# Performance work log

Measured on AMD Instinct MI355X. Metric: run time of the kernel, lower is better.

The kernel has to match this reference:

```python
import jax, jax.numpy as jnp
import numpy as np

EPS = 1e-5


def _in_relu(y):
    # instance norm (no affine, biased var, eps=1e-5) + ReLU, y: [B,C,H,W]
    mu = jnp.mean(y, axis=(-2, -1), keepdims=True)
    var = jnp.mean((y - mu) ** 2, axis=(-2, -1), keepdims=True)
    return jax.nn.relu((y - mu) * jax.lax.rsqrt(var + EPS))


def _conv3(x, w, b):
    # x: [C,H,W], w: [O,I,3,3] -> [O,H,W]
    y = jax.lax.conv_general_dilated(x[None], w, (1, 1), ((1, 1), (1, 1)),
                                     dimension_numbers=('NCHW', 'OIHW', 'NCHW'))[0]
    return y + b[:, None, None]


def _mod_block(x, W, b, mod):
    # per-sample weight modulation: mod[n] * W, then conv+IN+relu; x: [B,C,H,W], mod: [B,O,I,3,3]
    y = jax.vmap(lambda xi, mi: _conv3(xi, mi * W, b))(x, mod)
    return _in_relu(y)


def _maxpool2(x):
    return jax.lax.reduce_window(x, -jnp.inf, jax.lax.max, (1, 1, 2, 2), (1, 1, 2, 2), 'VALID')


def _up2(x):
    B, C, H, W = x.shape
    # bilinear, half-pixel centers == PyTorch align_corners=False
    return jax.image.resize(x, (B, C, 2 * H, 2 * W), method='bilinear')


def _conv1x1(x, w, b):
    y = jax.lax.conv_general_dilated(x, w, (1, 1), 'VALID',
                                     dimension_numbers=('NCHW', 'OIHW', 'NCHW'))
    return y + b[None, :, None, None]


def setup_inputs() -> dict:
    key = jax.random.key(0)
    B, H, W = 8, 256, 256
    ks = iter(jax.random.split(key, 64))
    d = {}
    d['us_query_input'] = jax.random.normal(next(ks), (B, 1, H, W), jnp.float32)
    d['ksp_query_imgs'] = jax.random.normal(next(ks), (B, H, W, 2), jnp.float32)
    d['ksp_mask_query'] = jax.random.uniform(next(ks), (B, H, W), jnp.float32)
    down_io = [(1, 32), (32, 64), (64, 128), (128, 256)]
    up_io = [(512, 128), (256, 64), (128, 32), (64, 32)]
    for i, (ci, co) in enumerate(down_io):
        d[f'down_mod_{i}'] = jax.random.normal(next(ks), (B, co, ci, 3, 3), jnp.float32)
        d[f'W_d{i}'] = 0.05 * jax.random.normal(next(ks), (co, ci, 3, 3), jnp.float32)
        d[f'b_d{i}'] = 0.05 * jax.random.normal(next(ks), (co,), jnp.float32)
    d['latent_mod'] = jax.random.normal(next(ks), (B, 256, 256, 3, 3), jnp.float32)
    d['W_lat'] = 0.05 * jax.random.normal(next(ks), (256, 256, 3, 3), jnp.float32)
    d['b_lat'] = 0.05 * jax.random.normal(next(ks), (256,), jnp.float32)
    for i, (ci, co) in enumerate(up_io):
        d[f'up_mod_{i}'] = jax.random.normal(next(ks), (B, co, ci, 3, 3), jnp.float32)
        d[f'W_u{i}'] = 0.05 * jax.random.normal(next(ks), (co, ci, 3, 3), jnp.float32)
        d[f'b_u{i}'] = 0.05 * jax.random.normal(next(ks), (co,), jnp.float32)
    d['w_c1'] = 0.05 * jax.random.normal(next(ks), (16, 32, 1, 1), jnp.float32)
    d['b_c1'] = 0.05 * jax.random.normal(next(ks), (16,), jnp.float32)
    d['w_c2'] = 0.05 * jax.random.normal(next(ks), (1, 16, 1, 1), jnp.float32)
    d['b_c2'] = 0.05 * jax.random.normal(next(ks), (1,), jnp.float32)
    d['w_c3'] = 0.05 * jax.random.normal(next(ks), (1, 1, 1, 1), jnp.float32)
    d['b_c3'] = 0.05 * jax.random.normal(next(ks), (1,), jnp.float32)
    return d


def reference(us_query_input, ksp_query_imgs, ksp_mask_query,
              down_mod_0, down_mod_1, down_mod_2, down_mod_3,
              latent_mod, up_mod_0, up_mod_1, up_mod_2, up_mod_3,
              W_d0, b_d0, W_d1, b_d1, W_d2, b_d2, W_d3, b_d3,
              W_lat, b_lat,
              W_u0, b_u0, W_u1, b_u1, W_u2, b_u2, W_u3, b_u3,
              w_c1, b_c1, w_c2, b_c2, w_c3, b_c3):
    x0 = us_query_input
    out = x0
    skips = []
    downs = [(W_d0, b_d0, down_mod_0), (W_d1, b_d1, down_mod_1),
             (W_d2, b_d2, down_mod_2), (W_d3, b_d3, down_mod_3)]
    for Wc, bc, m in downs:
        out = _mod_block(out, Wc, bc, m)
        skips.append(out)
        out = _maxpool2(out)
    out = _mod_block(out, W_lat, b_lat, latent_mod)
    ups = [(W_u0, b_u0, up_mod_0), (W_u1, b_u1, up_mod_1),
           (W_u2, b_u2, up_mod_2), (W_u3, b_u3, up_mod_3)]
    for Wc, bc, m in ups:
        out = _up2(out)
        out = jnp.concatenate([out, skips.pop()], axis=1)
        out = _mod_block(out, Wc, bc, m)
    out = _conv1x1(_conv1x1(_conv1x1(out, w_c1, b_c1), w_c2, b_c2), w_c3, b_c3)
    out = out + x0
    # FFT data consistency
    pred = out[:, 0]                                  # [B,H,W]
    kpred = jnp.fft.fft2(pred, norm='ortho')
    ksp = ksp_query_imgs[..., 0] + 1j * ksp_query_imgs[..., 1]
    upd = ksp_mask_query * ksp + (1.0 - ksp_mask_query) * kpred
    img = jnp.fft.ifft2(upd, norm='ortho')
    return jnp.real(img)[:, None].astype(jnp.float32)   # [B,1,H,W]
```

## Files before the change

### kernel.cpp

```cpp
#include <hip/hip_runtime.h>


#define EPS_IN 1e-5f

typedef __attribute__((ext_vector_type(8))) short short8;
typedef __attribute__((ext_vector_type(4))) short short4_t;
typedef __attribute__((ext_vector_type(4))) float f32x4;

__device__ __forceinline__ short f2bf(float f) {
    unsigned u = __float_as_uint(f);
    unsigned r = (u + 0x7fffu + ((u >> 16) & 1u)) >> 16;
    return (short)r;
}
__device__ __forceinline__ float bf2f(short s) {
    return __uint_as_float(((unsigned)(unsigned short)s) << 16);
}

__global__ void zero_f(float* __restrict__ p, int n)
{
    int i = blockIdx.x * 256 + threadIdx.x;
    if (i < n) p[i] = 0.f;
}

struct WmJobs {
    const float* W[8];
    const float* mod[8];
    short* wm[8];
    int Co[8];
    int Ci[8];
    int cum[9];
};

__global__ void make_wm_all(WmJobs j)
{
    int idx = blockIdx.x * 256 + threadIdx.x;
    if (idx >= j.cum[8]) return;
    int l = 0;
    while (idx >= j.cum[l + 1]) ++l;
    int local = idx - j.cum[l];
    const int Ci = j.Ci[l], Co = j.Co[l];
    int ci = local % Ci;
    int rem = local / Ci;
    int co = rem % Co;
    int b = rem / Co;
    const float* wp = j.W[l] + (size_t)(co * Ci + ci) * 9;
    const float* mp = j.mod[l] + ((size_t)((size_t)b * Co + co) * Ci + ci) * 9;
    short* wm = j.wm[l];
#pragma unroll
    for (int k = 0; k < 9; ++k)
        wm[(((size_t)(b * 9 + k) * Co + co) * Ci + ci)] = f2bf(wp[k] * mp[k]);
}

template <int VR, int NCOG, bool UP>
__global__ __launch_bounds__(256) void conv3x3_cl(
    const short* __restrict__ x1, int Ci1,
    const short* __restrict__ x2,
    const float2* __restrict__ st1, float invHW1,
    const short* __restrict__ wm,
    short* __restrict__ y,
    float2* __restrict__ stats,
    int Ci, int Co, int H, int W)
{
    constexpr int TH = 4 * VR, SH = TH + 2, SW = 18;
    constexpr int STN = UP ? 256 : 1;
    __shared__ short s_x[SH][SW][32];
    __shared__ float s_red[4][4][NCOG][4][2];
    __shared__ float2 s_st1[STN];

    const int tid = threadIdx.x;
    const int lane = tid & 63, wv = tid >> 6;
    const int m = lane & 15, g = lane >> 4;

    const int b = blockIdx.x & 7;
    int r = blockIdx.x >> 3;
    const int nCoB = Co / (16 * NCOG);
    const int coblk = r % nCoB;
    const int tileId = r / nCoB;
    const int tilesx = W >> 4;
    const int tx0 = (tileId % tilesx) * 16;
    const int ty0 = (tileId / tilesx) * TH;
    const int co0 = coblk * (16 * NCOG);
    const int Ci2 = Ci - Ci1;
    const int Hs = H >> 1, Ws = W >> 1;

    if (UP) {
        for (int i = tid; i < Ci1; i += 256) {
            float2 v = st1[(size_t)b * Ci1 + i];
            float mu = v.x * invHW1;
            float var = v.y * invHW1 - mu * mu;
            s_st1[i] = make_float2(mu, rsqrtf(var + EPS_IN));
        }
    }

    f32x4 acc[NCOG][VR];
#pragma unroll
    for (int cg = 0; cg < NCOG; ++cg)
#pragma unroll
        for (int rr = 0; rr < VR; ++rr) acc[cg][rr] = (f32x4)0.f;

    const short* wmb = wm + (size_t)b * 9 * Co * Ci;
    const short* x1b = x1 + (size_t)b * (UP ? (size_t)Hs * Ws : (size_t)H * W) * Ci1;
    const short* x2b = x2 + (size_t)b * H * W * Ci2;

    for (int ci0 = 0; ci0 < Ci; ci0 += 32) {
        __syncthreads();
        if (UP && ci0 < Ci1) {
            const int cb = ci0;
            for (int idx = tid; idx < SH * SW * 4; idx += 256) {
                int gg = idx & 3, pos = idx >> 2;
                int yy = pos / SW, xx = pos - yy * SW;
                int gy = ty0 + yy - 1, gx = tx0 + xx - 1;
                short8 v = (short8)0;
                if (gy >= 0 && gy < H && gx >= 0 && gx < W) {
                    int xk = gx >> 1, yk = gy >> 1;
                    int xo = gx & 1, yo = gy & 1;
                    int xa = xo ? xk : (xk > 0 ? xk - 1 : 0);
                    int xb = xo ? (xk + 1 < Ws ? xk + 1 : Ws - 1) : xk;
                    float wxa = xo ? 0.75f : 0.25f;
                    int ya = yo ? yk : (yk > 0 ? yk - 1 : 0);
                    int yb = yo ? (yk + 1 < Hs ? yk + 1 : Hs - 1) : yk;
                    float wya = yo ? 0.75f : 0.25f;
                    const short* ib = x1b + cb + gg * 8;
                    short8 vaa = *(const short8*)(ib + ((size_t)ya * Ws + xa) * Ci1);
                    short8 vab = *(const short8*)(ib + ((size_t)ya * Ws + xb) * Ci1);
                    short8 vba = *(const short8*)(ib + ((size_t)yb * Ws + xa) * Ci1);
                    short8 vbb = *(const short8*)(ib + ((size_t)yb * Ws + xb) * Ci1);
#pragma unroll
                    for (int e = 0; e < 8; ++e) {
                        float2 sv = s_st1[cb + gg * 8 + e];
                        float aa = fmaxf(0.f, (bf2f(vaa[e]) - sv.x) * sv.y);
                        float ab = fmaxf(0.f, (bf2f(vab[e]) - sv.x) * sv.y);
                        float ba = fmaxf(0.f, (bf2f(vba[e]) - sv.x) * sv.y);
                        float bb = fmaxf(0.f, (bf2f(vbb[e]) - sv.x) * sv.y);
                        float r0 = wxa * aa + (1.f - wxa) * ab;
                        float r1 = wxa * ba + (1.f - wxa) * bb;
                        v[e] = f2bf(wya * r0 + (1.f - wya) * r1);
                    }
                }
                *(short8*)&s_x[yy][xx][(gg ^ (xx & 3)) * 8] = v;
            }
        } else {
            const short* src; int C, cb;
            if (ci0 < Ci1) { src = x1b; C = Ci1; cb = ci0; }
            else           { src = x2b; C = Ci2; cb = ci0 - Ci1; }
            for (int idx = tid; idx < SH * SW * 4; idx += 256) {
                int gg = idx & 3, pos = idx >> 2;
                int yy = pos / SW, xx = pos - yy * SW;
                int gy = ty0 + yy - 1, gx = tx0 + xx - 1;
                short8 v = (short8)0;
                if (gy >= 0 && gy < H && gx >= 0 && gx < W)
                    v = *(const short8*)(src + ((size_t)gy * W + gx) * C + cb + gg * 8);
                *(short8*)&s_x[yy][xx][(gg ^ (xx & 3)) * 8] = v;
            }
        }
        __syncthreads();
#pragma unroll
        for (int t = 0; t < 9; ++t) {
            const int dy = t / 3, dx = t - 3 * (t / 3);
            const short* wr = wmb + ((size_t)t * Co + co0) * Ci + ci0 + g * 8;
            short8 a[NCOG];
#pragma unroll
            for (int cg = 0; cg < NCOG; ++cg)
                a[cg] = *(const short8*)(wr + (size_t)(cg * 16 + m) * Ci);
            const int xx = m + dx;
            const int sgo = (g ^ (xx & 3)) * 8;
#pragma unroll
            for (int rr = 0; rr < VR; ++rr) {
                short8 bf = *(const short8*)&s_x[wv * VR + rr + dy][xx][sgo];
#pragma unroll
                for (int cg = 0; cg < NCOG; ++cg)
                    acc[cg][rr] = __builtin_amdgcn_mfma_f32_16x16x32_bf16(a[cg], bf, acc[cg][rr], 0, 0, 0);
            }
        }
    }

    const int ox = tx0 + m;
#pragma unroll
    for (int cg = 0; cg < NCOG; ++cg)
#pragma unroll
        for (int rr = 0; rr < VR; ++rr) {
            int oy = ty0 + wv * VR + rr;
            short4_t o;
#pragma unroll
            for (int q = 0; q < 4; ++q) o[q] = f2bf(acc[cg][rr][q]);
            *(short4_t*)(y + (((size_t)b * H + oy) * W + ox) * Co + co0 + cg * 16 + g * 4) = o;
        }

#pragma unroll
    for (int cg = 0; cg < NCOG; ++cg)
#pragma unroll
        for (int q = 0; q < 4; ++q) {
            float s = 0.f, s2 = 0.f;
#pragma unroll
            for (int rr = 0; rr < VR; ++rr) { float v = acc[cg][rr][q]; s += v; s2 += v * v; }
#pragma unroll
            for (int msk = 1; msk < 16; msk <<= 1) { s += __shfl_xor(s, msk); s2 += __shfl_xor(s2, msk); }
            if (m == 0) { s_red[wv][g][cg][q][0] = s; s_red[wv][g][cg][q][1] = s2; }
        }
    __syncthreads();
    for (int i = tid; i < 16 * NCOG; i += 256) {
        int q = i & 3, gg = (i >> 2) & 3, cg = i >> 4;
        float S = 0.f, S2 = 0.f;
#pragma unroll
        for (int w = 0; w < 4; ++w) { S += s_red[w][gg][cg][q][0]; S2 += s_red[w][gg][cg][q][1]; }
        float* sp = (float*)&stats[(size_t)b * Co + co0 + i];
        atomicAdd(sp, S); atomicAdd(sp + 1, S2);
    }
}

__global__ __launch_bounds__(256) void conv_d0_cl(
    const float* __restrict__ x0, const float* __restrict__ W,
    const float* __restrict__ mod, short* __restrict__ y,
    float2* __restrict__ stats)
{
    __shared__ float s[18][18];
    __shared__ float sw[32][9];
    __shared__ float s_red[4][32][2];
    const int tid = threadIdx.x;
    const int tx = tid & 15, ty = tid >> 4;
    const int tx0 = (blockIdx.x & 15) * 16, ty0 = (blockIdx.x >> 4) * 16;
    const int b = blockIdx.y;
    if (tid < 288) sw[tid / 9][tid % 9] = W[tid] * mod[b * 288 + tid];
    for (int pos = tid; pos < 18 * 18; pos += 256) {
        int yy = pos / 18, xx = pos - yy * 18;
        int gy = ty0 + yy - 1, gx = tx0 + xx - 1;
        bool inb = gy >= 0 && gy < 256 && gx >= 0 && gx < 256;
        s[yy][xx] = inb ? x0[((size_t)b << 16) + gy * 256 + gx] : 0.f;
    }
    __syncthreads();
    float v[3][3];
#pragma unroll
    for (int r = 0; r < 3; ++r)
#pragma unroll
        for (int c = 0; c < 3; ++c) v[r][c] = s[ty + r][tx + c];
    float vals[32];
#pragma unroll
    for (int co = 0; co < 32; ++co) {
        float a = 0.f;
#pragma unroll
        for (int r = 0; r < 3; ++r)
#pragma unroll
            for (int c = 0; c < 3; ++c) a = fmaf(v[r][c], sw[co][r * 3 + c], a);
        vals[co] = a;
    }
    short* yp = y + (((size_t)b * 256 + ty0 + ty) * 256 + tx0 + tx) * 32;
#pragma unroll
    for (int j = 0; j < 4; ++j) {
        short8 o;
#pragma unroll
        for (int e = 0; e < 8; ++e) o[e] = f2bf(vals[j * 8 + e]);
        *(short8*)(yp + j * 8) = o;
    }
    const int lane = tid & 63, wv = tid >> 6;
#pragma unroll
    for (int co = 0; co < 32; ++co) {
        float sm = vals[co], s2 = vals[co] * vals[co];
#pragma unroll
        for (int off = 32; off > 0; off >>= 1) { sm += __shfl_down(sm, off); s2 += __shfl_down(s2, off); }
        if (lane == 0) { s_red[wv][co][0] = sm; s_red[wv][co][1] = s2; }
    }
    __syncthreads();
    if (tid < 32) {
        float S = 0.f, S2 = 0.f;
#pragma unroll
        for (int w = 0; w < 4; ++w) { S += s_red[w][tid][0]; S2 += s_red[w][tid][1]; }
        float* sp = (float*)&stats[(size_t)b * 32 + tid];
        atomicAdd(sp, S); atomicAdd(sp + 1, S2);
    }
}

__global__ void maxpool_cl(short* __restrict__ in,
                           const float2* __restrict__ st, float invHW,
                           short* __restrict__ out,
                           int c8s, int ws, int hs, int total8)
{
    const int C = 8 << c8s;
    for (int idx = blockIdx.x * 256 + threadIdx.x; idx < total8; idx += gridDim.x * 256) {
        int c8 = idx & ((1 << c8s) - 1);
        int p = idx >> c8s;
        int x = p & ((1 << ws) - 1);
        int yy = (p >> ws) & ((1 << hs) - 1);
        int b = p >> (ws + hs);
        short* ip = in + (((size_t)b * (2 << hs) + 2 * yy) * (2 << ws) + 2 * x) * C + c8 * 8;
        size_t rs = (size_t)(2 << ws) * C;
        short8 v0 = *(const short8*)ip, v1 = *(const short8*)(ip + C);
        short8 v2 = *(const short8*)(ip + rs), v3 = *(const short8*)(ip + rs + C);
        short8 o, w0, w1, w2, w3;
#pragma unroll
        for (int e = 0; e < 8; ++e) {
            float2 sv = st[(size_t)b * C + c8 * 8 + e];
            float mu = sv.x * invHW;
            float rsig = rsqrtf(sv.y * invHW - mu * mu + EPS_IN);
            float n0 = fmaxf(0.f, (bf2f(v0[e]) - mu) * rsig);
            float n1 = fmaxf(0.f, (bf2f(v1[e]) - mu) * rsig);
            float n2 = fmaxf(0.f, (bf2f(v2[e]) - mu) * rsig);
            float n3 = fmaxf(0.f, (bf2f(v3[e]) - mu) * rsig);
            w0[e] = f2bf(n0); w1[e] = f2bf(n1); w2[e] = f2bf(n2); w3[e] = f2bf(n3);
            o[e] = f2bf(fmaxf(fmaxf(n0, n1), fmaxf(n2, n3)));
        }
        *(short8*)ip = w0;
        *(short8*)(ip + C) = w1;
        *(short8*)(ip + rs) = w2;
        *(short8*)(ip + rs + C) = w3;
        *(short8*)(out + (size_t)idx * 8) = o;
    }
}

__global__ void eff1x1(const float* __restrict__ w1, const float* __restrict__ b1,
                       const float* __restrict__ w2, const float* __restrict__ b2,
                       const float* __restrict__ w3, const float* __restrict__ b3,
                       float* __restrict__ eff)
{
    int t = threadIdx.x;
    if (t < 32) {
        float s = 0.f;
        for (int k = 0; k < 16; ++k) s += w2[k] * w1[k * 32 + t];
        eff[t] = w3[0] * s;
    }
    if (t == 32) {
        float s = 0.f;
        for (int k = 0; k < 16; ++k) s += w2[k] * b1[k];
        eff[32] = w3[0] * (s + b2[0]) + b3[0];
    }
}

__device__ __forceinline__ void fft256(float2* s, int tid, float sign)
{
    __syncthreads();
#pragma unroll
    for (int t = 0; t < 4; ++t) {
        int i = tid + t * 64;
        int r = __brev(i) >> 24;
        if (r > i) { float2 tmp = s[i]; s[i] = s[r]; s[r] = tmp; }
    }
    __syncthreads();
    for (int st = 1; st <= 8; ++st) {
        int m = 1 << st, half = m >> 1;
#pragma unroll
        for (int t = 0; t < 2; ++t) {
            int k = tid + t * 64;
            int g = k >> (st - 1), j = k & (half - 1);
            int i0 = (g << st) + j, i1 = i0 + half;
            float ang = sign * 6.283185307179586f * (float)j / (float)m;
            float sn, cs;
            __sincosf(ang, &sn, &cs);
            float2 a = s[i0], b = s[i1];
            float2 tt = make_float2(b.x * cs - b.y * sn, b.x * sn + b.y * cs);
            s[i0] = make_float2(a.x + tt.x, a.y + tt.y);
            s[i1] = make_float2(a.x - tt.x, a.y - tt.y);
        }
        __syncthreads();
    }
}

__global__ __launch_bounds__(64) void final_fft_rows(
    const short* __restrict__ act, const float2* __restrict__ st, float invHW,
    const float* __restrict__ x0, const float* __restrict__ eff,
    float2* __restrict__ cplx)
{
    __shared__ float2 s[256];
    __shared__ float2 sst[32];
    __shared__ float seff[33];
    const int row = blockIdx.x, tid = threadIdx.x;
    const int b = row >> 8, yy = row & 255;
    if (tid < 32) {
        float2 v = st[(size_t)b * 32 + tid];
        float mu = v.x * invHW;
        sst[tid] = make_float2(mu, rsqrtf(v.y * invHW - mu * mu + EPS_IN));
    }
    if (tid < 33) seff[tid] = eff[tid];
    __syncthreads();
#pragma unroll
    for (int k = 0; k < 4; ++k) {
        int x = k * 64 + tid;
        const short8* a = (const short8*)(act + (((size_t)b * 256 + yy) * 256 + x) * 32);
        float sacc = seff[32] + x0[((size_t)b << 16) + (yy << 8) + x];
#pragma unroll
        for (int j = 0; j < 4; ++j) {
            short8 v = a[j];
#pragma unroll
            for (int e = 0; e < 8; ++e) {
                float2 sv = sst[j * 8 + e];
                sacc += seff[j * 8 + e] * fmaxf(0.f, (bf2f(v[e]) - sv.x) * sv.y);
            }
        }
        s[x] = make_float2(sacc, 0.f);
    }
    fft256(s, tid, -1.f);
    float2* o = cplx + (size_t)row * 256;
    for (int i = tid; i < 256; i += 64) o[i] = s[i];
}

__global__ __launch_bounds__(64) void fft_cols_combine(float2* __restrict__ data,
                                                       const float* __restrict__ ksp,
                                                       const float* __restrict__ mask)
{
    __shared__ float2 s[256];
    int col = blockIdx.x & 255, b = blockIdx.x >> 8;
    int tid = threadIdx.x;
    float2* base = data + (size_t)b * 65536 + col;
    for (int i = tid; i < 256; i += 64) s[i] = base[(size_t)i * 256];
    fft256(s, tid, -1.f);
    for (int i = tid; i < 256; i += 64) {
        size_t mi = ((size_t)b * 256 + i) * 256 + col;
        float m = mask[mi];
        float2 kp = s[i];
        float kr = ksp[mi * 2], ki = ksp[mi * 2 + 1];
        s[i] = make_float2(m * kr + (1.f - m) * kp.x * (1.f / 256.f),
                           m * ki + (1.f - m) * kp.y * (1.f / 256.f));
    }
    fft256(s, tid, 1.f);
    for (int i = tid; i < 256; i += 64) base[(size_t)i * 256] = s[i];
}

__global__ __launch_bounds__(64) void fft_rows_inv(const float2* __restrict__ data,
                                                   float* __restrict__ out)
{
    __shared__ float2 s[256];
    int row = blockIdx.x, tid = threadIdx.x;
    const float2* p = data + (size_t)row * 256;
    for (int i = tid; i < 256; i += 64) s[i] = p[i];
    fft256(s, tid, 1.f);
    float* o = out + (size_t)row * 256;
    for (int i = tid; i < 256; i += 64) o[i] = s[i].x * (1.f / 256.f);
}

extern "C" void kernel_launch(void* const* d_in, const int* in_sizes, int n_in,
                              void* d_out, int out_size, void* d_ws, size_t ws_size,
                              hipStream_t stream)
{
    (void)in_sizes; (void)n_in; (void)out_size; (void)ws_size;

    const float* x0 = (const float*)d_in[0];
    const float* ksp = (const float*)d_in[1];
    const float* mask = (const float*)d_in[2];
    const float* mod_d[4] = {(const float*)d_in[3], (const float*)d_in[6],
                             (const float*)d_in[9], (const float*)d_in[12]};
    const float* W_d[4] = {(const float*)d_in[4], (const float*)d_in[7],
                           (const float*)d_in[10], (const float*)d_in[13]};
    const float* mod_lat = (const float*)d_in[15];
    const float* W_lat = (const float*)d_in[16];
    const float* mod_u[4] = {(const float*)d_in[18], (const float*)d_in[21],
                             (const float*)d_in[24], (const float*)d_in[27]};
    const float* W_u[4] = {(const float*)d_in[19], (const float*)d_in[22],
                           (const float*)d_in[25], (const float*)d_in[28]};
    const float* w_c1 = (const float*)d_in[30];
    const float* b_c1 = (const float*)d_in[31];
    const float* w_c2 = (const float*)d_in[32];
    const float* b_c2 = (const float*)d_in[33];
    const float* w_c3 = (const float*)d_in[34];
    const float* b_c3 = (const float*)d_in[35];

    short* sA  = (short*)d_ws;
    short* sB  = sA + 16777216;
    short* sk0 = sB + 16777216;
    short* sk1 = sk0 + 16777216;
    short* sk2 = sk1 + 8388608;
    short* sk3 = sk2 + 4194304;
    short* wm_d1 = sk3 + 2097152;
    short* wm_d2 = wm_d1 + 147456;
    short* wm_d3 = wm_d2 + 589824;
    short* wm_lat = wm_d3 + 2359296;
    short* wm_u0 = wm_lat + 4718592;
    short* wm_u1 = wm_u0 + 4718592;
    short* wm_u2 = wm_u1 + 1179648;
    short* wm_u3 = wm_u2 + 294912;
    float2* cplx = (float2*)(wm_u3 + 147456);
    float2* stA = cplx + 524288;
    float* eff = (float*)(stA + 7936);

    float2* st_d0 = stA + 0;
    float2* st_d1 = stA + 256;
    float2* st_d2 = stA + 768;
    float2* st_d3 = stA + 1792;
    float2* st_lat = stA + 3840;
    float2* st_u0 = stA + 5888;
    float2* st_u1 = stA + 6912;
    float2* st_u2 = stA + 7424;
    float2* st_u3 = stA + 7680;

    const float i64k = 1.f / 65536.f, i16k = 1.f / 16384.f, i4k = 1.f / 4096.f,
                i1k = 1.f / 1024.f, i256 = 1.f / 256.f;

    dim3 blk(256);

    zero_f<<<62, blk, 0, stream>>>((float*)stA, 15872);
    eff1x1<<<1, 64, 0, stream>>>(w_c1, b_c1, w_c2, b_c2, w_c3, b_c3, eff);

    WmJobs jobs;
    const float* Wl[8]  = {W_d[1], W_d[2], W_d[3], W_lat, W_u[0], W_u[1], W_u[2], W_u[3]};
    const float* Ml[8]  = {mod_d[1], mod_d[2], mod_d[3], mod_lat, mod_u[0], mod_u[1], mod_u[2], mod_u[3]};
    short* WMl[8] = {wm_d1, wm_d2, wm_d3, wm_lat, wm_u0, wm_u1, wm_u2, wm_u3};
    int Col[8] = {64, 128, 256, 256, 128, 64, 32, 32};
    int Cil[8] = {32, 64, 128, 256, 512, 256, 128, 64};
    jobs.cum[0] = 0;
    for (int l = 0; l < 8; ++l) {
        jobs.W[l] = Wl[l]; jobs.mod[l] = Ml[l]; jobs.wm[l] = WMl[l];
        jobs.Co[l] = Col[l]; jobs.Ci[l] = Cil[l];
        jobs.cum[l + 1] = jobs.cum[l] + 8 * Col[l] * Cil[l];
    }
    make_wm_all<<<(jobs.cum[8] + 255) / 256, blk, 0, stream>>>(jobs);

    conv_d0_cl<<<dim3(256, 8), blk, 0, stream>>>(x0, W_d[0], mod_d[0], sk0, st_d0);
    maxpool_cl<<<2048, blk, 0, stream>>>(sk0, st_d0, i64k, sA, 2, 7, 7, 524288);

    conv3x3_cl<4, 4, false><<<512, blk, 0, stream>>>(sA, 32, sA, stA, 0.f, wm_d1, sk1, st_d1, 32, 64, 128, 128);
    maxpool_cl<<<1024, blk, 0, stream>>>(sk1, st_d1, i16k, sA, 3, 6, 6, 262144);

    conv3x3_cl<2, 4, false><<<512, blk, 0, stream>>>(sA, 64, sA, stA, 0.f, wm_d2, sk2, st_d2, 64, 128, 64, 64);
    maxpool_cl<<<512, blk, 0, stream>>>(sk2, st_d2, i4k, sA, 4, 5, 5, 131072);

    conv3x3_cl<2, 2, false><<<512, blk, 0, stream>>>(sA, 128, sA, stA, 0.f, wm_d3, sk3, st_d3, 128, 256, 32, 32);
    maxpool_cl<<<256, blk, 0, stream>>>(sk3, st_d3, i1k, sA, 5, 4, 4, 65536);

    conv3x3_cl<2, 1, false><<<256, blk, 0, stream>>>(sA, 256, sA, stA, 0.f, wm_lat, sB, st_lat, 256, 256, 16, 16);

    conv3x3_cl<2, 1, true><<<512, blk, 0, stream>>>(sB, 256, sk3, st_lat, i256, wm_u0, sA, st_u0, 512, 128, 32, 32);
    conv3x3_cl<2, 2, true><<<512, blk, 0, stream>>>(sA, 128, sk2, st_u0, i1k, wm_u1, sB, st_u1, 256, 64, 64, 64);
    conv3x3_cl<4, 2, true><<<512, blk, 0, stream>>>(sB, 64, sk1, st_u1, i4k, wm_u2, sA, st_u2, 128, 32, 128, 128);
    conv3x3_cl<4, 2, true><<<2048, blk, 0, stream>>>(sA, 32, sk0, st_u2, i16k, wm_u3, sB, st_u3, 64, 32, 256, 256);

    final_fft_rows<<<2048, 64, 0, stream>>>(sB, st_u3, i64k, x0, eff, cplx);

    fft_cols_combine<<<2048, 64, 0, stream>>>(cplx, ksp, mask);
    fft_rows_inv<<<2048, 64, 0, stream>>>(cplx, (float*)d_out);
}
```

Before: 501.8 us.

## Stage conv outputs through LDS for coalesced stores and pre-upsample latent

Conv3x3 and the first-layer conv now write their bf16 outputs into shared memory first, then copy them out with 16-byte contiguous stores instead of scattered 8-byte per-lane writes. A separate upsample kernel applies the instance-norm, ReLU and bilinear upsampling to the latent output, so the first up-conv runs on the non-UP path instead of doing the fused upsample in its input loading. This adds barriers and LDS traffic plus an extra kernel launch and an extra buffer pass, in exchange for better write coalescing and simpler input loads.

```diff
diff --git a/kernel.cpp b/kernel.cpp
--- a/kernel.cpp
+++ b/kernel.cpp
@@ -63,7 +63,8 @@
 {
     constexpr int TH = 4 * VR, SH = TH + 2, SW = 18;
     constexpr int STN = UP ? 256 : 1;
-    __shared__ short s_x[SH][SW][32];
+    constexpr bool DW = (TH * 16 * NCOG * 16 * 2) <= (SH * SW * 32 * 2);
+    __shared__ __align__(16) short s_x[SH][SW][32];
     __shared__ float s_red[4][4][NCOG][4][2];
     __shared__ float2 s_st1[STN];
 
@@ -174,17 +175,42 @@
         }
     }
 
-    const int ox = tx0 + m;
-#pragma unroll
-    for (int cg = 0; cg < NCOG; ++cg)
-#pragma unroll
-        for (int rr = 0; rr < VR; ++rr) {
-            int oy = ty0 + wv * VR + rr;
-            short4_t o;
-#pragma unroll
-            for (int q = 0; q < 4; ++q) o[q] = f2bf(acc[cg][rr][q]);
-            *(short4_t*)(y + (((size_t)b * H + oy) * W + ox) * Co + co0 + cg * 16 + g * 4) = o;
-        }
+    if constexpr (DW) {
+        __syncthreads();
+        short* sd = (short*)&s_x[0][0][0];
+#pragma unroll
+        for (int cg = 0; cg < NCOG; ++cg)
+#pragma unroll
+            for (int rr = 0; rr < VR; ++rr) {
+                short4_t o;
+#pragma unroll
+                for (int q = 0; q < 4; ++q) o[q] = f2bf(acc[cg][rr][q]);
+                *(short4_t*)&sd[((wv * VR + rr) * 16 + m) * (NCOG * 16) + cg * 16 + g * 4] = o;
+            }
+        __syncthreads();
+        constexpr int N16 = TH * 16 * NCOG * 2;
+        constexpr int CPR = NCOG * 32;
+        for (int c = tid; c < N16; c += 256) {
+            int row = c / CPR;
+            int o16 = c % CPR;
+            int p = o16 / (NCOG * 2);
+            int cw = o16 % (NCOG * 2);
+            short8 v = *(short8*)&sd[(row * 16 + p) * (NCOG * 16) + cw * 8];
+            *(short8*)(y + (((size_t)b * H + ty0 + row) * W + tx0 + p) * Co + co0 + cw * 8) = v;
+        }
+    } else {
+        const int ox = tx0 + m;
+#pragma unroll
+        for (int cg = 0; cg < NCOG; ++cg)
+#pragma unroll
+            for (int rr = 0; rr < VR; ++rr) {
+                int oy = ty0 + wv * VR + rr;
+                short4_t o;
+#pragma unroll
+                for (int q = 0; q < 4; ++q) o[q] = f2bf(acc[cg][rr][q]);
+                *(short4_t*)(y + (((size_t)b * H + oy) * W + ox) * Co + co0 + cg * 16 + g * 4) = o;
+            }
+    }
 
 #pragma unroll
     for (int cg = 0; cg < NCOG; ++cg)
@@ -216,6 +242,7 @@
     __shared__ float s[18][18];
     __shared__ float sw[32][9];
     __shared__ float s_red[4][32][2];
+    __shared__ __align__(16) short sd[16][16][32];
     const int tid = threadIdx.x;
     const int tx = tid & 15, ty = tid >> 4;
     const int tx0 = (blockIdx.x & 15) * 16, ty0 = (blockIdx.x >> 4) * 16;
@@ -243,13 +270,12 @@
             for (int c = 0; c < 3; ++c) a = fmaf(v[r][c], sw[co][r * 3 + c], a);
         vals[co] = a;
     }
-    short* yp = y + (((size_t)b * 256 + ty0 + ty) * 256 + tx0 + tx) * 32;
 #pragma unroll
     for (int j = 0; j < 4; ++j) {
         short8 o;
 #pragma unroll
         for (int e = 0; e < 8; ++e) o[e] = f2bf(vals[j * 8 + e]);
-        *(short8*)(yp + j * 8) = o;
+        *(short8*)&sd[ty][tx][j * 8] = o;
     }
     const int lane = tid & 63, wv = tid >> 6;
 #pragma unroll
@@ -260,6 +286,11 @@
         if (lane == 0) { s_red[wv][co][0] = sm; s_red[wv][co][1] = s2; }
     }
     __syncthreads();
+    for (int c = tid; c < 1024; c += 256) {
+        int row = c >> 6, o = c & 63;
+        short8 vv = *(short8*)&sd[row][o >> 2][(o & 3) * 8];
+        *(short8*)(y + (((size_t)b * 256 + ty0 + row) * 256 + tx0 + (o >> 2)) * 32 + (o & 3) * 8) = vv;
+    }
     if (tid < 32) {
         float S = 0.f, S2 = 0.f;
 #pragma unroll
@@ -302,6 +333,49 @@
         *(short8*)(ip + C) = w1;
         *(short8*)(ip + rs) = w2;
         *(short8*)(ip + rs + C) = w3;
+        *(short8*)(out + (size_t)idx * 8) = o;
+    }
+}
+
+__global__ void upsample_cl(const short* __restrict__ in,
+                            const float2* __restrict__ st, float invHW,
+                            short* __restrict__ out,
+                            int c8s, int wsi, int hsi, int total8)
+{
+    const int C = 8 << c8s;
+    const int Win = 1 << wsi, Hin = 1 << hsi;
+    for (int idx = blockIdx.x * 256 + threadIdx.x; idx < total8; idx += gridDim.x * 256) {
+        int c8 = idx & ((1 << c8s) - 1);
+        int p = idx >> c8s;
+        int x = p & (2 * Win - 1);
+        int yy = (p >> (wsi + 1)) & (2 * Hin - 1);
+        int b = p >> (wsi + 1 + hsi + 1);
+        int xk = x >> 1, yk = yy >> 1;
+        int xa, xb; float wxa;
+        if (x & 1) { xa = xk; xb = (xk + 1 < Win) ? xk + 1 : Win - 1; wxa = 0.75f; }
+        else       { xa = (xk > 0) ? xk - 1 : 0; xb = xk; wxa = 0.25f; }
+        int ya, yb; float wya;
+        if (yy & 1) { ya = yk; yb = (yk + 1 < Hin) ? yk + 1 : Hin - 1; wya = 0.75f; }
+        else        { ya = (yk > 0) ? yk - 1 : 0; yb = yk; wya = 0.25f; }
+        const short* ib = in + (size_t)b * Hin * Win * C + c8 * 8;
+        short8 vaa = *(const short8*)(ib + ((size_t)ya * Win + xa) * C);
+        short8 vab = *(const short8*)(ib + ((size_t)ya * Win + xb) * C);
+        short8 vba = *(const short8*)(ib + ((size_t)yb * Win + xa) * C);
+        short8 vbb = *(const short8*)(ib + ((size_t)yb * Win + xb) * C);
+        short8 o;
+#pragma unroll
+        for (int e = 0; e < 8; ++e) {
+            float2 sv = st[(size_t)b * C + c8 * 8 + e];
+            float mu = sv.x * invHW;
+            float rsig = rsqrtf(sv.y * invHW - mu * mu + EPS_IN);
+            float aa = fmaxf(0.f, (bf2f(vaa[e]) - mu) * rsig);
+            float ab = fmaxf(0.f, (bf2f(vab[e]) - mu) * rsig);
+            float ba = fmaxf(0.f, (bf2f(vba[e]) - mu) * rsig);
+            float bb = fmaxf(0.f, (bf2f(vbb[e]) - mu) * rsig);
+            float r0 = wxa * aa + (1.f - wxa) * ab;
+            float r1 = wxa * ba + (1.f - wxa) * bb;
+            o[e] = f2bf(wya * r0 + (1.f - wya) * r1);
+        }
         *(short8*)(out + (size_t)idx * 8) = o;
     }
 }
@@ -515,12 +589,13 @@
 
     conv3x3_cl<2, 1, false><<<256, blk, 0, stream>>>(sA, 256, sA, stA, 0.f, wm_lat, sB, st_lat, 256, 256, 16, 16);
 
-    conv3x3_cl<2, 1, true><<<512, blk, 0, stream>>>(sB, 256, sk3, st_lat, i256, wm_u0, sA, st_u0, 512, 128, 32, 32);
-    conv3x3_cl<2, 2, true><<<512, blk, 0, stream>>>(sA, 128, sk2, st_u0, i1k, wm_u1, sB, st_u1, 256, 64, 64, 64);
-    conv3x3_cl<4, 2, true><<<512, blk, 0, stream>>>(sB, 64, sk1, st_u1, i4k, wm_u2, sA, st_u2, 128, 32, 128, 128);
-    conv3x3_cl<4, 2, true><<<2048, blk, 0, stream>>>(sA, 32, sk0, st_u2, i16k, wm_u3, sB, st_u3, 64, 32, 256, 256);
-
-    final_fft_rows<<<2048, 64, 0, stream>>>(sB, st_u3, i64k, x0, eff, cplx);
+    upsample_cl<<<1024, blk, 0, stream>>>(sB, st_lat, i256, sA, 5, 4, 4, 262144);
+    conv3x3_cl<2, 1, false><<<512, blk, 0, stream>>>(sA, 256, sk3, stA, 0.f, wm_u0, sB, st_u0, 512, 128, 32, 32);
+    conv3x3_cl<2, 2, true><<<512, blk, 0, stream>>>(sB, 128, sk2, st_u0, i1k, wm_u1, sA, st_u1, 256, 64, 64, 64);
+    conv3x3_cl<4, 2, true><<<512, blk, 0, stream>>>(sA, 64, sk1, st_u1, i4k, wm_u2, sB, st_u2, 128, 32, 128, 128);
+    conv3x3_cl<4, 2, true><<<2048, blk, 0, stream>>>(sB, 32, sk0, st_u2, i16k, wm_u3, sA, st_u3, 64, 32, 256, 256);
+
+    final_fft_rows<<<2048, 64, 0, stream>>>(sA, st_u3, i64k, x0, eff, cplx);
 
     fft_cols_combine<<<2048, 64, 0, stream>>>(cplx, ksp, mask);
     fft_rows_inv<<<2048, 64, 0, stream>>>(cplx, (float*)d_out);
```

Result: no change. 496.1 us (-1.1%).
